# Kernel optimization log

Hardware: AMD Instinct MI355X
Metric: run time of the kernel (lower is better)

The kernel has to match this reference:

```python
import jax, jax.numpy as jnp
import numpy as np

EPS = 1e-10

def setup_inputs() -> dict:
    key = jax.random.key(0)
    k1, k2 = jax.random.split(key)
    support_set = jax.random.normal(k1, (8192, 1024), dtype=jnp.float32)
    input_image = jax.random.normal(k2, (2048, 1024), dtype=jnp.float32)
    return {"support_set": support_set, "input_image": input_image}

def reference(support_set, input_image):
    # support_set: [n, d], input_image: [b, d]
    # Faithful to original: input magnitude is a single scalar over the whole
    # [b, d] input matrix; support magnitude is a scalar per support vector.
    input_mag = jax.lax.rsqrt(jnp.maximum(jnp.sum(input_image * input_image), EPS))  # scalar
    support_mag = jax.lax.rsqrt(jnp.maximum(jnp.sum(support_set * support_set, axis=1), EPS))  # [n]
    dot = jnp.einsum('bd,nd->nb', input_image, support_set)  # [n, b]
    sims = dot * support_mag[:, None] * input_mag  # [n, b]
    return sims[:, :, None]  # [n, b, 1] == torch.stack(...)[n,b,1].squeeze(1) (no-op for b>1)
```

## Files before the change

kernel.cpp:

```cpp
#include <hip/hip_runtime.h>
#include <hip/hip_bf16.h>
#include <stdint.h>
#include <stddef.h>

#define M_DIM 8192
#define N_DIM 2048
#define K_DIM 1024

#define BM 256
#define BN 256
#define BK 64
#define NKT (K_DIM / BK)
#define NITER (NKT / 2)

typedef __attribute__((ext_vector_type(8))) short short8;
typedef __attribute__((ext_vector_type(4))) float float4v;

static __device__ __forceinline__ unsigned short f2bf(float x) {
  union { float f; unsigned u; } c; c.f = x;
  return (unsigned short)((c.u + 0x7FFFu + ((c.u >> 16) & 1u)) >> 16);
}

#define GLOAD_LDS16(g, l)                                           \
  __builtin_amdgcn_global_load_lds(                                 \
      (const __attribute__((address_space(1))) void*)(g),           \
      (__attribute__((address_space(3))) void*)(l), 16, 0, 0)

__global__ __launch_bounds__(256) void prep(
    const float* __restrict__ S, const float* __restrict__ I,
    unsigned short* __restrict__ Sb, unsigned short* __restrict__ Ib,
    float* __restrict__ smag, float* __restrict__ partials) {
  const int t = threadIdx.x;
  const int blk = blockIdx.x;
  const bool isS = blk < M_DIM;
  const int row = isS ? blk : blk - M_DIM;
  const float* src = (isS ? S : I) + (size_t)row * K_DIM;
  unsigned short* dst = (isS ? Sb : Ib) + (size_t)row * K_DIM;

  const float4 v = reinterpret_cast<const float4*>(src)[t];
  ushort4 b;
  b.x = f2bf(v.x); b.y = f2bf(v.y); b.z = f2bf(v.z); b.w = f2bf(v.w);
  reinterpret_cast<ushort4*>(dst)[t] = b;

  float ss = v.x * v.x + v.y * v.y + v.z * v.z + v.w * v.w;
#pragma unroll
  for (int m = 32; m >= 1; m >>= 1) ss += __shfl_xor(ss, m, 64);
  __shared__ float wsum[4];
  if ((t & 63) == 0) wsum[t >> 6] = ss;
  __syncthreads();
  if (t == 0) {
    const float tot = wsum[0] + wsum[1] + wsum[2] + wsum[3];
    if (isS) smag[row] = rsqrtf(fmaxf(tot, 1e-10f));
    else     partials[row] = tot;
  }
}

__global__ __launch_bounds__(512, 2) void gemm_bt(
    const unsigned short* __restrict__ A,
    const unsigned short* __restrict__ B,
    const float* __restrict__ smag,
    const float* __restrict__ partials,
    float* __restrict__ C) {
  __shared__ __align__(16) unsigned short lA[32768];
  __shared__ __align__(16) unsigned short lB[32768];
  __shared__ float wsum[8];

  const int t = threadIdx.x;
  const int lane = t & 63;
  const int wave = t >> 6;
  const int wr = wave >> 2;
  const int wc = wave & 3;

  const int blk = blockIdx.x;
  const int xcd = blk & 7;
  const int slot = blk >> 3;
  const int bm = (xcd * 4 + (slot & 3)) * BM;
  const int bn = (slot >> 2) * BN;

  {
    float p = partials[t] + partials[t + 512] + partials[t + 1024] + partials[t + 1536];
#pragma unroll
    for (int m = 32; m >= 1; m >>= 1) p += __shfl_xor(p, m, 64);
    if (lane == 0) wsum[wave] = p;
  }

  const int srow = t >> 3;
  const int skc = (t & 7) ^ (srow & 7);
  const unsigned short* gA[4];
  const unsigned short* gB[4];
  int aoff[4];
#pragma unroll
  for (int j = 0; j < 4; ++j) {
    gA[j] = A + (size_t)(bm + j * 64 + srow) * K_DIM + skc * 8;
    gB[j] = B + (size_t)(bn + j * 64 + srow) * K_DIM + skc * 8;
    aoff[j] = (j >> 1) * 8192 + (j & 1) * 4096 + wave * 512;
  }

#define STAGE_A(j, buf) do { GLOAD_LDS16(gA[j], &lA[(buf) * 16384 + aoff[j]]); gA[j] += BK; } while (0)
#define STAGE_B(j, buf) do { GLOAD_LDS16(gB[j], &lB[(buf) * 16384 + aoff[j]]); gB[j] += BK; } while (0)
#define SP1(buf) do { STAGE_B(0, buf); STAGE_B(1, buf); } while (0)
#define SP2(buf) do { STAGE_B(2, buf); STAGE_B(3, buf); } while (0)
#define SP3(buf) do { STAGE_A(0, buf); STAGE_A(2, buf); } while (0)
#define SP4(buf) do { STAGE_A(1, buf); STAGE_A(3, buf); } while (0)

  const int fr = lane & 15;
  const int q = lane >> 4;
  const int pc0 = (q ^ (fr & 7)) * 8;
  const int pc1 = ((4 + q) ^ (fr & 7)) * 8;
  const unsigned short* rA = lA + wr * 8192 + fr * 64;
  const unsigned short* rB = lB + (wc >> 1) * 8192 + ((wc & 1) * 64 + fr) * 64;

  short8 af[2][2];
  short8 bf[4][2];
  float4v acc[8][4];
#pragma unroll
  for (int i = 0; i < 8; ++i)
#pragma unroll
    for (int j = 0; j < 4; ++j) acc[i][j] = (float4v)0.0f;

#define BARRIER() __builtin_amdgcn_s_barrier()
#define LGKM0() asm volatile("s_waitcnt lgkmcnt(0)" ::: "memory")
#define VM6() asm volatile("s_waitcnt vmcnt(6)" ::: "memory")
#define VM0() asm volatile("s_waitcnt vmcnt(0)" ::: "memory")
#define PRIO1() __builtin_amdgcn_s_setprio(1)
#define PRIO0() __builtin_amdgcn_s_setprio(0)

#define LOADB(buf) do {                                                        \
    _Pragma("unroll") for (int nj = 0; nj < 4; ++nj) {                         \
      bf[nj][0] = *reinterpret_cast<const short8*>(rB + (buf) * 16384 + nj * 1024 + pc0); \
      bf[nj][1] = *reinterpret_cast<const short8*>(rB + (buf) * 16384 + nj * 1024 + pc1); \
    } } while (0)

#define LOADA(pi, buf) do {                                                    \
    _Pragma("unroll") for (int m2 = 0; m2 < 2; ++m2) {                         \
      af[m2][0] = *reinterpret_cast<const short8*>(rA + (buf) * 16384 + ((pi) * 2 + m2) * 1024 + pc0); \
      af[m2][1] = *reinterpret_cast<const short8*>(rA + (buf) * 16384 + ((pi) * 2 + m2) * 1024 + pc1); \
    } } while (0)

#define MFMA16(pi) do {                                                        \
    _Pragma("unroll") for (int m2 = 0; m2 < 2; ++m2)                           \
    _Pragma("unroll") for (int nj = 0; nj < 4; ++nj) {                         \
      acc[(pi) * 2 + m2][nj] = __builtin_amdgcn_mfma_f32_16x16x32_bf16(        \
          af[m2][0], bf[nj][0], acc[(pi) * 2 + m2][nj], 0, 0, 0);              \
      acc[(pi) * 2 + m2][nj] = __builtin_amdgcn_mfma_f32_16x16x32_bf16(        \
          af[m2][1], bf[nj][1], acc[(pi) * 2 + m2][nj], 0, 0, 0);              \
    } } while (0)

#define ITER(DS) do {                                                          \
                                                   \
    LOADB(0); LOADA(0, 0); SP4(1);                                             \
    BARRIER(); LGKM0(); PRIO1(); MFMA16(0); PRIO0(); BARRIER();                \
                                                         \
    LOADA(1, 0); if (DS) SP1(0);                                               \
    BARRIER(); LGKM0(); PRIO1(); MFMA16(1); PRIO0(); BARRIER();                \
                                                         \
    LOADA(2, 0); if (DS) SP2(0);                                               \
    BARRIER(); LGKM0(); PRIO1(); MFMA16(2); PRIO0(); BARRIER();                \
                                         \
    LOADA(3, 0); if (DS) SP3(0);                                               \
    if (DS) { VM6(); } else { VM0(); }                                         \
    BARRIER(); LGKM0(); PRIO1(); MFMA16(3); PRIO0(); BARRIER();                \
                                                   \
    LOADB(1); LOADA(0, 1); if (DS) SP4(0);                                     \
    BARRIER(); LGKM0(); PRIO1(); MFMA16(0); PRIO0(); BARRIER();                \
                                                         \
    LOADA(1, 1); if (DS) SP1(1);                                               \
    BARRIER(); LGKM0(); PRIO1(); MFMA16(1); PRIO0(); BARRIER();                \
                                                         \
    LOADA(2, 1); if (DS) SP2(1);                                               \
    BARRIER(); LGKM0(); PRIO1(); MFMA16(2); PRIO0(); BARRIER();                \
                                         \
    LOADA(3, 1); if (DS) SP3(1);                                               \
    if (DS) { VM6(); }                                                         \
    BARRIER(); LGKM0(); PRIO1(); MFMA16(3); PRIO0(); BARRIER();                \
  } while (0)

  SP1(0); SP2(0); SP3(0); SP4(0);
  SP1(1); SP2(1); SP3(1);
  VM6();
  BARRIER();

#pragma unroll 1
  for (int it = 0; it < NITER - 1; ++it) ITER(1);
  ITER(0);

  const float imag = rsqrtf(fmaxf(wsum[0] + wsum[1] + wsum[2] + wsum[3] +
                                  wsum[4] + wsum[5] + wsum[6] + wsum[7], 1e-10f));
#pragma unroll
  for (int mi = 0; mi < 8; ++mi) {
    const int rbase = bm + wr * 128 + mi * 16 + q * 4;
#pragma unroll
    for (int r = 0; r < 4; ++r) {
      const int row = rbase + r;
      const float sc = smag[row] * imag;
      float* crow = C + (size_t)row * N_DIM + bn + wc * 64 + fr;
#pragma unroll
      for (int nj = 0; nj < 4; ++nj) crow[nj * 16] = acc[mi][nj][r] * sc;
    }
  }
}

extern "C" void kernel_launch(void* const* d_in, const int* in_sizes, int n_in,
                              void* d_out, int out_size, void* d_ws, size_t ws_size,
                              hipStream_t stream) {
  const float* S = (const float*)d_in[0];
  const float* I = (const float*)d_in[1];
  float* out = (float*)d_out;

  unsigned char* ws = (unsigned char*)d_ws;
  unsigned short* Sb = (unsigned short*)ws;
  unsigned short* Ib = (unsigned short*)(ws + (size_t)M_DIM * K_DIM * 2);
  float* smag = (float*)(ws + (size_t)M_DIM * K_DIM * 2 + (size_t)N_DIM * K_DIM * 2);
  float* partials = smag + M_DIM;

  hipLaunchKernelGGL(prep, dim3(M_DIM + N_DIM), dim3(256), 0, stream,
                     S, I, Sb, Ib, smag, partials);
  hipLaunchKernelGGL(gemm_bt, dim3((M_DIM / BM) * (N_DIM / BN)), dim3(512), 0, stream,
                     Sb, Ib, smag, partials, out);
}
```

Before: 127.9 us.

## Double-buffer LDS fragment registers in GEMM and use one wave per row in prep

The GEMM main loop now keeps two register banks for the A and B fragments. The LDS reads for the next sub-tile are issued right after each barrier, before the MFMAs of the current sub-tile, so the lgkmcnt(0) stall before each MFMA block goes away and the vmcnt waits are retuned. The prep kernel now has each wave handle one full row, removing the shared-memory reduction and __syncthreads, and launches four times fewer blocks. The price is higher register pressure from the duplicated fragment banks, which could cause spills or lower occupancy. Correctness of the LDS reads now depends on the compiler-inserted waits and the barrier placement.

New measurement: 126.9 us. About the same (-0.7%).

```diff
diff --git a/kernel.cpp b/kernel.cpp
--- a/kernel.cpp
+++ b/kernel.cpp
@@ -31,27 +31,28 @@
     unsigned short* __restrict__ Sb, unsigned short* __restrict__ Ib,
     float* __restrict__ smag, float* __restrict__ partials) {
   const int t = threadIdx.x;
+  const int lane = t & 63;
+  const int wave = t >> 6;
   const int blk = blockIdx.x;
-  const bool isS = blk < M_DIM;
-  const int row = isS ? blk : blk - M_DIM;
+  const bool isS = blk < 2048;
+  const int row = (isS ? blk : blk - 2048) * 4 + wave;
   const float* src = (isS ? S : I) + (size_t)row * K_DIM;
   unsigned short* dst = (isS ? Sb : Ib) + (size_t)row * K_DIM;
 
-  const float4 v = reinterpret_cast<const float4*>(src)[t];
-  ushort4 b;
-  b.x = f2bf(v.x); b.y = f2bf(v.y); b.z = f2bf(v.z); b.w = f2bf(v.w);
-  reinterpret_cast<ushort4*>(dst)[t] = b;
-
-  float ss = v.x * v.x + v.y * v.y + v.z * v.z + v.w * v.w;
+  float ss = 0.f;
+#pragma unroll
+  for (int i = 0; i < 4; ++i) {
+    const float4 v = reinterpret_cast<const float4*>(src)[lane + i * 64];
+    ushort4 b;
+    b.x = f2bf(v.x); b.y = f2bf(v.y); b.z = f2bf(v.z); b.w = f2bf(v.w);
+    reinterpret_cast<ushort4*>(dst)[lane + i * 64] = b;
+    ss += v.x * v.x + v.y * v.y + v.z * v.z + v.w * v.w;
+  }
 #pragma unroll
   for (int m = 32; m >= 1; m >>= 1) ss += __shfl_xor(ss, m, 64);
-  __shared__ float wsum[4];
-  if ((t & 63) == 0) wsum[t >> 6] = ss;
-  __syncthreads();
-  if (t == 0) {
-    const float tot = wsum[0] + wsum[1] + wsum[2] + wsum[3];
-    if (isS) smag[row] = rsqrtf(fmaxf(tot, 1e-10f));
-    else     partials[row] = tot;
+  if (lane == 0) {
+    if (isS) smag[row] = rsqrtf(fmaxf(ss, 1e-10f));
+    else     partials[row] = ss;
   }
 }
 
@@ -83,6 +84,7 @@
     for (int m = 32; m >= 1; m >>= 1) p += __shfl_xor(p, m, 64);
     if (lane == 0) wsum[wave] = p;
   }
+  asm volatile("s_waitcnt vmcnt(0)" ::: "memory");
 
   const int srow = t >> 3;
   const int skc = (t & 7) ^ (srow & 7);
@@ -110,8 +112,8 @@
   const unsigned short* rA = lA + wr * 8192 + fr * 64;
   const unsigned short* rB = lB + (wc >> 1) * 8192 + ((wc & 1) * 64 + fr) * 64;
 
-  short8 af[2][2];
-  short8 bf[4][2];
+  short8 af0[2][2], af1[2][2];
+  short8 bfA[4][2], bfB[4][2];
   float4v acc[8][4];
 #pragma unroll
   for (int i = 0; i < 8; ++i)
@@ -119,70 +121,78 @@
     for (int j = 0; j < 4; ++j) acc[i][j] = (float4v)0.0f;
 
 #define BARRIER() __builtin_amdgcn_s_barrier()
-#define LGKM0() asm volatile("s_waitcnt lgkmcnt(0)" ::: "memory")
-#define VM6() asm volatile("s_waitcnt vmcnt(6)" ::: "memory")
-#define VM0() asm volatile("s_waitcnt vmcnt(0)" ::: "memory")
+#define VMW(n) asm volatile("s_waitcnt vmcnt(" #n ")" ::: "memory")
 #define PRIO1() __builtin_amdgcn_s_setprio(1)
 #define PRIO0() __builtin_amdgcn_s_setprio(0)
 
-#define LOADB(buf) do {                                                        \
+#define LOADB(bank, buf) do {                                                  \
     _Pragma("unroll") for (int nj = 0; nj < 4; ++nj) {                         \
-      bf[nj][0] = *reinterpret_cast<const short8*>(rB + (buf) * 16384 + nj * 1024 + pc0); \
-      bf[nj][1] = *reinterpret_cast<const short8*>(rB + (buf) * 16384 + nj * 1024 + pc1); \
+      bank[nj][0] = *reinterpret_cast<const short8*>(rB + (buf) * 16384 + nj * 1024 + pc0); \
+      bank[nj][1] = *reinterpret_cast<const short8*>(rB + (buf) * 16384 + nj * 1024 + pc1); \
     } } while (0)
 
-#define LOADA(pi, buf) do {                                                    \
+#define LOADA(bank, buf, pi) do {                                              \
     _Pragma("unroll") for (int m2 = 0; m2 < 2; ++m2) {                         \
-      af[m2][0] = *reinterpret_cast<const short8*>(rA + (buf) * 16384 + ((pi) * 2 + m2) * 1024 + pc0); \
-      af[m2][1] = *reinterpret_cast<const short8*>(rA + (buf) * 16384 + ((pi) * 2 + m2) * 1024 + pc1); \
+      bank[m2][0] = *reinterpret_cast<const short8*>(rA + (buf) * 16384 + ((pi) * 2 + m2) * 1024 + pc0); \
+      bank[m2][1] = *reinterpret_cast<const short8*>(rA + (buf) * 16384 + ((pi) * 2 + m2) * 1024 + pc1); \
     } } while (0)
 
-#define MFMA16(pi) do {                                                        \
+#define MFMA16(pi, abank, bbank) do {                                          \
     _Pragma("unroll") for (int m2 = 0; m2 < 2; ++m2)                           \
     _Pragma("unroll") for (int nj = 0; nj < 4; ++nj) {                         \
       acc[(pi) * 2 + m2][nj] = __builtin_amdgcn_mfma_f32_16x16x32_bf16(        \
-          af[m2][0], bf[nj][0], acc[(pi) * 2 + m2][nj], 0, 0, 0);              \
+          abank[m2][0], bbank[nj][0], acc[(pi) * 2 + m2][nj], 0, 0, 0);        \
       acc[(pi) * 2 + m2][nj] = __builtin_amdgcn_mfma_f32_16x16x32_bf16(        \
-          af[m2][1], bf[nj][1], acc[(pi) * 2 + m2][nj], 0, 0, 0);              \
+          abank[m2][1], bbank[nj][1], acc[(pi) * 2 + m2][nj], 0, 0, 0);        \
     } } while (0)
 
-#define ITER(DS) do {                                                          \
-                                                   \
-    LOADB(0); LOADA(0, 0); SP4(1);                                             \
-    BARRIER(); LGKM0(); PRIO1(); MFMA16(0); PRIO0(); BARRIER();                \
-                                                         \
-    LOADA(1, 0); if (DS) SP1(0);                                               \
-    BARRIER(); LGKM0(); PRIO1(); MFMA16(1); PRIO0(); BARRIER();                \
-                                                         \
-    LOADA(2, 0); if (DS) SP2(0);                                               \
-    BARRIER(); LGKM0(); PRIO1(); MFMA16(2); PRIO0(); BARRIER();                \
-                                         \
-    LOADA(3, 0); if (DS) SP3(0);                                               \
-    if (DS) { VM6(); } else { VM0(); }                                         \
-    BARRIER(); LGKM0(); PRIO1(); MFMA16(3); PRIO0(); BARRIER();                \
-                                                   \
-    LOADB(1); LOADA(0, 1); if (DS) SP4(0);                                     \
-    BARRIER(); LGKM0(); PRIO1(); MFMA16(0); PRIO0(); BARRIER();                \
-                                                         \
-    LOADA(1, 1); if (DS) SP1(1);                                               \
-    BARRIER(); LGKM0(); PRIO1(); MFMA16(1); PRIO0(); BARRIER();                \
-                                                         \
-    LOADA(2, 1); if (DS) SP2(1);                                               \
-    BARRIER(); LGKM0(); PRIO1(); MFMA16(2); PRIO0(); BARRIER();                \
-                                         \
-    LOADA(3, 1); if (DS) SP3(1);                                               \
-    if (DS) { VM6(); }                                                         \
-    BARRIER(); LGKM0(); PRIO1(); MFMA16(3); PRIO0(); BARRIER();                \
+#define ITER_F() do {                                                          \
+     SP4(1);           BARRIER(); LOADA(af1, 0, 1);                   \
+              PRIO1(); MFMA16(0, af0, bfA); PRIO0();                           \
+     SP1(0); VMW(10);  BARRIER(); LOADA(af0, 0, 2);                   \
+              PRIO1(); MFMA16(1, af1, bfA); PRIO0();                           \
+     SP2(0);           BARRIER(); LOADA(af1, 0, 3);                   \
+              PRIO1(); MFMA16(2, af0, bfA); PRIO0();                           \
+     SP3(0); VMW(8);   BARRIER(); LOADB(bfB, 1); LOADA(af0, 1, 0);    \
+              PRIO1(); MFMA16(3, af1, bfA); PRIO0();                           \
+     SP4(0);           BARRIER(); LOADA(af1, 1, 1);                   \
+              PRIO1(); MFMA16(0, af0, bfB); PRIO0();                           \
+     SP1(1); VMW(10);  BARRIER(); LOADA(af0, 1, 2);                   \
+              PRIO1(); MFMA16(1, af1, bfB); PRIO0();                           \
+     SP2(1);           BARRIER(); LOADA(af1, 1, 3);                   \
+              PRIO1(); MFMA16(2, af0, bfB); PRIO0();                           \
+     SP3(1); VMW(8);   BARRIER(); LOADB(bfA, 0); LOADA(af0, 0, 0);    \
+              PRIO1(); MFMA16(3, af1, bfB); PRIO0();                           \
+  } while (0)
+
+#define ITER_T() do {                                                          \
+     SP4(1);           BARRIER(); LOADA(af1, 0, 1);                   \
+              PRIO1(); MFMA16(0, af0, bfA); PRIO0();                           \
+     VMW(8);           BARRIER(); LOADA(af0, 0, 2);                   \
+              PRIO1(); MFMA16(1, af1, bfA); PRIO0();                           \
+                       BARRIER(); LOADA(af1, 0, 3);                   \
+              PRIO1(); MFMA16(2, af0, bfA); PRIO0();                           \
+     VMW(2);           BARRIER(); LOADB(bfB, 1); LOADA(af0, 1, 0);    \
+              PRIO1(); MFMA16(3, af1, bfA); PRIO0();                           \
+                       BARRIER(); LOADA(af1, 1, 1);                   \
+              PRIO1(); MFMA16(0, af0, bfB); PRIO0();                           \
+     VMW(0);           BARRIER(); LOADA(af0, 1, 2);                   \
+              PRIO1(); MFMA16(1, af1, bfB); PRIO0();                           \
+                       BARRIER(); LOADA(af1, 1, 3);                   \
+              PRIO1(); MFMA16(2, af0, bfB); PRIO0();                           \
+                       BARRIER();                                     \
+              PRIO1(); MFMA16(3, af1, bfB); PRIO0();                           \
   } while (0)
 
   SP1(0); SP2(0); SP3(0); SP4(0);
   SP1(1); SP2(1); SP3(1);
-  VM6();
+  VMW(6);
   BARRIER();
+  LOADB(bfA, 0); LOADA(af0, 0, 0);
 
 #pragma unroll 1
-  for (int it = 0; it < NITER - 1; ++it) ITER(1);
-  ITER(0);
+  for (int it = 0; it < NITER - 1; ++it) ITER_F();
+  ITER_T();
 
   const float imag = rsqrtf(fmaxf(wsum[0] + wsum[1] + wsum[2] + wsum[3] +
                                   wsum[4] + wsum[5] + wsum[6] + wsum[7], 1e-10f));
@@ -213,7 +223,7 @@
   float* smag = (float*)(ws + (size_t)M_DIM * K_DIM * 2 + (size_t)N_DIM * K_DIM * 2);
   float* partials = smag + M_DIM;
 
-  hipLaunchKernelGGL(prep, dim3(M_DIM + N_DIM), dim3(256), 0, stream,
+  hipLaunchKernelGGL(prep, dim3(2560), dim3(256), 0, stream,
                      S, I, Sb, Ib, smag, partials);
   hipLaunchKernelGGL(gemm_bt, dim3((M_DIM / BM) * (N_DIM / BN)), dim3(512), 0, stream,
                      Sb, Ib, smag, partials, out);
```
